# Kernel tuning notes

Measured on AMD Instinct MI355X. Metric: run time of the kernel, lower is better.

## Reference

```python
import jax, jax.numpy as jnp
import numpy as np

B, S, D, H, HD, L, E, K, F = 1, 1024, 1024, 16, 64, 64, 8, 2, 4096
EPS = 1e-6


def rms_norm(x):
    return x / jnp.sqrt(jnp.mean(x * x, axis=-1, keepdims=True) + EPS)


def rope_sincos(seq, dim):
    # standard GPT-NeoX-style rotary tables, shape [seq, dim]
    inv = 1.0 / (10000.0 ** (jnp.arange(0, dim, 2, dtype=jnp.float32) / dim))
    ang = jnp.arange(seq, dtype=jnp.float32)[:, None] * inv[None, :]
    sin = jnp.concatenate([jnp.sin(ang), jnp.sin(ang)], axis=-1)
    cos = jnp.concatenate([jnp.cos(ang), jnp.cos(ang)], axis=-1)
    return sin, cos


def apply_rotary(x, sin, cos):
    d = x.shape[-1] // 2
    rot = jnp.concatenate([-x[..., d:], x[..., :d]], axis=-1)
    return x * cos + rot * sin


def setup_inputs() -> dict:
    key = jax.random.key(0)
    ks = jax.random.split(key, 16)
    sd = 0.02

    def nrm(k, shp):
        return jax.random.normal(k, shp, jnp.float32) * sd

    return dict(
        x=jax.random.normal(ks[0], (B, S, D), jnp.float32),
        noise_u=jax.random.uniform(ks[1], (B, S, E), jnp.float32),
        Wdkv=nrm(ks[2], (H, L, HD)),      # per-head w_dkv  (torch weight [L,HD])
        Wq=nrm(ks[3], (H, HD, HD)),       # per-head wq
        Wuv=nrm(ks[4], (H, L, HD)),       # per-head w_uv
        Wuk=nrm(ks[5], (H, L, HD)),       # per-head w_uk
        Wk_rope=nrm(ks[6], (H, L, HD)),   # per-head w_k_rope
        Wq_rope=nrm(ks[7], (H, HD, L)),   # per-head w_q_rope weight
        bq_rope=jnp.zeros((H, HD), jnp.float32),  # w_q_rope bias (Linear default bias=True)
        Wo_head=nrm(ks[8], (H, HD, HD)),  # per-head w_o (no bias)
        Wr=nrm(ks[9], (E, D)),            # router weight
        Wn=nrm(ks[10], (E, D)),           # noise weight
        r_bias=jnp.zeros((E,), jnp.float32),
        W1=nrm(ks[11], (E, D, F)),        # expert fc1 (transposed torch layout)
        b1=jnp.zeros((E, F), jnp.float32),
        W2=nrm(ks[12], (E, F, D)),        # expert fc2
        b2=jnp.zeros((E, D), jnp.float32),
    )


def reference(x, noise_u, Wdkv, Wq, Wuv, Wuk, Wk_rope, Wq_rope, bq_rope,
              Wo_head, Wr, Wn, r_bias, W1, b1, W2, b2):
    # ---- multi-head latent attention (vectorized over heads) ----
    y = rms_norm(x)
    xs = y.reshape(B, S, H, HD).transpose(0, 2, 1, 3)  # [B,H,S,HD]
    sin_k, cos_k = rope_sincos(S, L)
    sin_q, cos_q = rope_sincos(S, HD)

    k = apply_rotary(jnp.einsum('bhsd,hld->bhsl', xs, Wk_rope), sin_k, cos_k)  # [B,H,S,L]
    ckv = jnp.einsum('bhsd,hld->bhsl', xs, Wdkv)                               # [B,H,S,L]
    q = jnp.einsum('bhsl,hdl->bhsd', ckv, Wq_rope) + bq_rope[None, :, None, :]
    q = apply_rotary(q, sin_q, cos_q)                                          # [B,H,S,HD]

    absorbed = jnp.einsum('hqe,hle->hql', Wq, Wuk)                             # [H,HD,L]
    s1 = jnp.einsum('bhsd,hdl,bhtl->bhst', xs, absorbed, ckv)
    s2 = jnp.einsum('bhsd,bhtd->bhst', q, k)
    scores = (s1 + s2) / jnp.sqrt(jnp.float32(2 * HD))
    mask = jnp.tril(jnp.ones((S, S), dtype=bool))  # past_length = 0
    scores = jnp.where(mask, scores, -jnp.inf)
    attn = jax.nn.softmax(scores, axis=-1)

    v = jnp.einsum('bhsl,hld->bhsd', ckv, Wuv)
    o = jnp.einsum('bhst,bhtd->bhsd', attn, v)
    o = jnp.einsum('bhsd,hed->bhse', o, Wo_head)  # per-head w_o (no bias)
    attn_out = o.transpose(0, 2, 1, 3).reshape(B, S, D)
    x = x + attn_out

    # ---- noisy top-k MoE ----
    y2 = rms_norm(x)
    logits = jnp.einsum('bsd,ed->bse', y2, Wr)
    noisy = jnp.einsum('bsd,ed->bse', y2, Wn)
    nl = noise_u * jax.nn.softplus(noisy) + logits + r_bias
    topv, topi = jax.lax.top_k(nl, K)
    gates = jax.nn.softmax(topv, axis=-1)  # softmax over -inf-scattered logits == softmax over top-k
    probs = jnp.sum(gates[..., None] * jax.nn.one_hot(topi, E, dtype=x.dtype), axis=-2)  # [B,S,E]

    h = jax.nn.gelu(jnp.einsum('bsd,edf->ebsf', y2, W1) + b1[:, None, None, :], approximate=False)
    eo = jnp.einsum('ebsf,efd->ebsd', h, W2) + b2[:, None, None, :]
    moe_out = jnp.einsum('bse,ebsd->bsd', probs, eo)
    return x + moe_out
```

## Files before the change

kernel.cpp:

```cpp
#include <hip/hip_runtime.h>
#include <math.h>

#define S_ 1024
#define D_ 1024
#define H_ 16
#define F_ 4096

typedef short s16x8 __attribute__((ext_vector_type(8)));
typedef float fx4 __attribute__((ext_vector_type(4)));

__device__ __forceinline__ float bf2f(unsigned int u){
  union { float f; unsigned int u; } v; v.u = u<<16; return v.f;
}
__device__ __forceinline__ unsigned short f2bf(float f){
  union { float f; unsigned int u; } v; v.f = f;
  unsigned int r = v.u + 0x7fffu + ((v.u>>16)&1u);
  return (unsigned short)(r>>16);
}
__device__ __forceinline__ unsigned int pk2(float a, float b){
  return (unsigned int)f2bf(a) | ((unsigned int)f2bf(b)<<16);
}
__device__ __forceinline__ void gld16(const void* g, void* l){
  typedef const unsigned int __attribute__((address_space(1)))* gp_t;
  typedef unsigned int __attribute__((address_space(3)))* lp_t;
  __builtin_amdgcn_global_load_lds((gp_t)g, (lp_t)l, 16, 0, 0);
}

__global__ __launch_bounds__(256) void k_rmsnorm(const float* __restrict__ x, unsigned short* __restrict__ y){
  int row = blockIdx.x, t = threadIdx.x;
  const float4 v = ((const float4*)(x + (size_t)row*D_))[t];
  float ss = v.x*v.x + v.y*v.y + v.z*v.z + v.w*v.w;
  #pragma unroll
  for(int o=1;o<64;o<<=1) ss += __shfl_xor(ss, o);
  __shared__ float red[4];
  if((t&63)==0) red[t>>6]=ss;
  __syncthreads();
  float sc = rsqrtf((red[0]+red[1]+red[2]+red[3])*(1.0f/D_) + 1e-6f);
  ushort4 o4;
  o4.x=f2bf(v.x*sc); o4.y=f2bf(v.y*sc); o4.z=f2bf(v.z*sc); o4.w=f2bf(v.w*sc);
  ((ushort4*)(y + (size_t)row*D_))[t]=o4;
}

__global__ __launch_bounds__(256) void k_prep(const float* __restrict__ Wq,
    const float* __restrict__ Wuk, const float* __restrict__ Wuv,
    float* __restrict__ abs_t, float* __restrict__ wuvt){
  int h = blockIdx.x, tid = threadIdx.x;
  __shared__ float wq[4096], wuk[4096];
  for(int i=tid;i<4096;i+=256){ wq[i]=Wq[h*4096+i]; wuk[i]=Wuk[h*4096+i]; }
  __syncthreads();
  for(int i=tid;i<4096;i+=256){
    float a=0.f;
    #pragma unroll 8
    for(int e=0;e<64;e++) a += wq[(i&63)*64+e]*wuk[(i>>6)*64+e];
    abs_t[h*4096+i]=a;
    wuvt[h*4096+i]=Wuv[h*4096 + (i&63)*64 + (i>>6)];
  }
}

__device__ __forceinline__ void stage_B64(const float* __restrict__ W, unsigned short* Bs, int tid){
  int n = tid>>2, kq = tid&3;
  const float* s = W + n*64 + kq*16;
  float4 f0=*(const float4*)(s), f1=*(const float4*)(s+4), f2=*(const float4*)(s+8), f3=*(const float4*)(s+12);
  ushort4 u0,u1,u2,u3;
  u0.x=f2bf(f0.x);u0.y=f2bf(f0.y);u0.z=f2bf(f0.z);u0.w=f2bf(f0.w);
  u1.x=f2bf(f1.x);u1.y=f2bf(f1.y);u1.z=f2bf(f1.z);u1.w=f2bf(f1.w);
  u2.x=f2bf(f2.x);u2.y=f2bf(f2.y);u2.z=f2bf(f2.z);u2.w=f2bf(f2.w);
  u3.x=f2bf(f3.x);u3.y=f2bf(f3.y);u3.z=f2bf(f3.z);u3.w=f2bf(f3.w);
  int sl0=((kq*2)^(n&7))*8, sl1=((kq*2+1)^(n&7))*8;
  *(ushort4*)&Bs[n*64+sl0]=u0;   *(ushort4*)&Bs[n*64+sl0+4]=u1;
  *(ushort4*)&Bs[n*64+sl1]=u2;   *(ushort4*)&Bs[n*64+sl1+4]=u3;
}
__device__ __forceinline__ void gemm64(const unsigned short* Asrc, const unsigned short* Bs,
    int wv, int l16, int l4, fx4 acc[4]){
  int srow = wv*16 + l16;
  #pragma unroll
  for(int kb=0;kb<2;kb++){
    s16x8 af = *(const s16x8*)&Asrc[srow*64 + (((kb*4+l4)^(srow&7))*8)];
    #pragma unroll
    for(int nf=0;nf<4;nf++){
      int n = nf*16+l16;
      s16x8 bf = *(const s16x8*)&Bs[n*64 + (((kb*4+l4)^(n&7))*8)];
      acc[nf] = __builtin_amdgcn_mfma_f32_16x16x32_bf16(af, bf, acc[nf], 0,0,0);
    }
  }
}

__global__ __launch_bounds__(256) void k_proj_m(const unsigned short* __restrict__ y,
    const float* __restrict__ abs_t, const float* __restrict__ wuvt,
    const float* __restrict__ Wdkv, const float* __restrict__ Wk_rope,
    const float* __restrict__ Wq_rope, const float* __restrict__ bq_rope,
    unsigned short* __restrict__ kk, unsigned short* __restrict__ qq,
    unsigned short* __restrict__ vv){
  __shared__ unsigned short ysd[4096];
  __shared__ unsigned short ckvs[4096];
  __shared__ unsigned short Bs[4096];
  __shared__ unsigned short tmp[64*72];
  const float LNC = 0.28782313662425575f;
  const float ASC = 0.08838834764831845f;
  int s0 = blockIdx.x*64, h = blockIdx.y, tid = threadIdx.x;
  int wv = tid>>6, lane = tid&63, l16 = lane&15, l4 = lane>>4;
  fx4 acc[4];

  {
    int rg = lane>>3, sg = (lane&7)^(rg&7);
    #pragma unroll
    for(int c2=0;c2<2;c2++){
      int c = wv*2+c2;
      gld16(y + (size_t)(s0+c*8+rg)*D_ + h*64 + sg*8, &ysd[c*512]);
    }
  }
  stage_B64(Wdkv + h*4096, Bs, tid);
  __syncthreads();

  #pragma unroll
  for(int nf=0;nf<4;nf++){acc[nf][0]=0.f;acc[nf][1]=0.f;acc[nf][2]=0.f;acc[nf][3]=0.f;}
  gemm64(ysd, Bs, wv, l16, l4, acc);
  #pragma unroll
  for(int nf=0;nf<4;nf++){
    int col = nf*16+l16;
    #pragma unroll
    for(int r=0;r<4;r++){
      int srow = wv*16+4*l4+r;
      ckvs[srow*64 + (((col>>3)^(srow&7))*8) + (col&7)] = f2bf(acc[nf][r]);
    }
  }
  __syncthreads();
  {
    int row=tid>>2, sl=(tid&3)*2;
    uint4 a=*(const uint4*)&ckvs[row*64+sl*8];
    uint4 b=*(const uint4*)&ckvs[row*64+sl*8+8];
    unsigned short* kr = kk + ((size_t)(h*S_)+s0+row)*128;
    *(uint4*)&kr[(sl^(row&7))*8]=a;
    *(uint4*)&kr[((sl+1)^(row&7))*8]=b;
  }
  stage_B64(Wk_rope + h*4096, Bs, tid);
  __syncthreads();

  #pragma unroll
  for(int nf=0;nf<4;nf++){acc[nf][0]=0.f;acc[nf][1]=0.f;acc[nf][2]=0.f;acc[nf][3]=0.f;}
  gemm64(ysd, Bs, wv, l16, l4, acc);
  #pragma unroll
  for(int nf=0;nf<2;nf++){
    int llo = nf*16+l16;
    float inv = __expf(-(float)llo * LNC);
    #pragma unroll
    for(int r=0;r<4;r++){
      int srow = wv*16+4*l4+r;
      float sn,cs; __sincosf((float)(s0+srow)*inv,&sn,&cs);
      float alo=acc[nf][r], ahi=acc[nf+2][r];
      tmp[srow*72 + llo]      = f2bf(alo*cs - ahi*sn);
      tmp[srow*72 + llo + 32] = f2bf(ahi*cs + alo*sn);
    }
  }
  __syncthreads();
  { int row=tid>>2, c=(tid&3)*16;
    uint4 a=*(const uint4*)&tmp[row*72+c]; uint4 b=*(const uint4*)&tmp[row*72+c+8];
    unsigned short* kr = kk + ((size_t)(h*S_)+s0+row)*128 + 64;
    *(uint4*)&kr[c]=a; *(uint4*)&kr[c+8]=b; }
  stage_B64(Wq_rope + h*4096, Bs, tid);
  __syncthreads();

  #pragma unroll
  for(int nf=0;nf<4;nf++){acc[nf][0]=0.f;acc[nf][1]=0.f;acc[nf][2]=0.f;acc[nf][3]=0.f;}
  gemm64(ckvs, Bs, wv, l16, l4, acc);
  #pragma unroll
  for(int nf=0;nf<4;nf++){
    float bq = bq_rope[h*64 + nf*16+l16];
    #pragma unroll
    for(int r=0;r<4;r++) acc[nf][r]+=bq;
  }
  #pragma unroll
  for(int nf=0;nf<2;nf++){
    int dlo = nf*16+l16;
    float inv = __expf(-(float)dlo * LNC);
    #pragma unroll
    for(int r=0;r<4;r++){
      int srow = wv*16+4*l4+r;
      float sn,cs; __sincosf((float)(s0+srow)*inv,&sn,&cs);
      float alo=acc[nf][r]*ASC, ahi=acc[nf+2][r]*ASC;
      tmp[srow*72 + dlo]      = f2bf(alo*cs - ahi*sn);
      tmp[srow*72 + dlo + 32] = f2bf(ahi*cs + alo*sn);
    }
  }
  __syncthreads();
  { int row=tid>>2, c=(tid&3)*16;
    uint4 a=*(const uint4*)&tmp[row*72+c]; uint4 b=*(const uint4*)&tmp[row*72+c+8];
    unsigned short* qr = qq + ((size_t)(h*S_)+s0+row)*128 + 64;
    *(uint4*)&qr[c]=a; *(uint4*)&qr[c+8]=b; }
  stage_B64(abs_t + h*4096, Bs, tid);
  __syncthreads();

  #pragma unroll
  for(int nf=0;nf<4;nf++){acc[nf][0]=0.f;acc[nf][1]=0.f;acc[nf][2]=0.f;acc[nf][3]=0.f;}
  gemm64(ysd, Bs, wv, l16, l4, acc);
  #pragma unroll
  for(int nf=0;nf<4;nf++)
    #pragma unroll
    for(int r=0;r<4;r++)
      tmp[(wv*16+4*l4+r)*72 + nf*16+l16] = f2bf(acc[nf][r]*ASC);
  __syncthreads();
  { int row=tid>>2, c=(tid&3)*16;
    uint4 a=*(const uint4*)&tmp[row*72+c]; uint4 b=*(const uint4*)&tmp[row*72+c+8];
    unsigned short* qr = qq + ((size_t)(h*S_)+s0+row)*128;
    *(uint4*)&qr[c]=a; *(uint4*)&qr[c+8]=b; }
  stage_B64(wuvt + h*4096, Bs, tid);
  __syncthreads();

  #pragma unroll
  for(int nf=0;nf<4;nf++){acc[nf][0]=0.f;acc[nf][1]=0.f;acc[nf][2]=0.f;acc[nf][3]=0.f;}
  gemm64(ckvs, Bs, wv, l16, l4, acc);
  #pragma unroll
  for(int nf=0;nf<4;nf++)
    #pragma unroll
    for(int r=0;r<4;r++)
      tmp[(wv*16+4*l4+r)*72 + nf*16+l16] = f2bf(acc[nf][r]);
  __syncthreads();
  { int row=tid>>2, c=(tid&3)*16;
    uint4 a=*(const uint4*)&tmp[row*72+c]; uint4 b=*(const uint4*)&tmp[row*72+c+8];
    unsigned short* vr = vv + ((size_t)(h*S_)+s0+row)*64;
    *(uint4*)&vr[c]=a; *(uint4*)&vr[c+8]=b; }
}

__global__ __launch_bounds__(256) void k_attn2(const unsigned short* __restrict__ qq,
    const unsigned short* __restrict__ kk, const unsigned short* __restrict__ vv,
    const float* __restrict__ Wo, const float* __restrict__ x, float* __restrict__ x1){
  __shared__ unsigned short Ks[64*128];
  __shared__ unsigned short Vt[64*72];
  __shared__ unsigned short Pl[4][16*72];
  int h = blockIdx.y, q0 = blockIdx.x*64, tid = threadIdx.x;
  int wave = tid>>6, lane = tid&63;
  int l16 = lane&15, l4 = lane>>4;
  int qglob = q0 + wave*16 + l16;

  s16x8 qf[4];
  {
    const unsigned short* qp = qq + ((size_t)(h*S_)+qglob)*128 + l4*8;
    #pragma unroll
    for(int kb=0;kb<4;kb++) qf[kb] = *(const s16x8*)(qp + kb*32);
  }
  fx4 ot[4];
  #pragma unroll
  for(int t=0;t<4;t++){ ot[t][0]=0.f; ot[t][1]=0.f; ot[t][2]=0.f; ot[t][3]=0.f; }
  float mrun=-1e30f, lrun=0.f;
  int nkt = blockIdx.x + 1;

  for(int kt=0;kt<nkt;kt++){
    int kt0 = kt*64;
    __syncthreads();
    #pragma unroll
    for(int it=0;it<4;it++){
      int idx = tid + it*256;
      int row = idx>>4, c = idx&15;
      uint4 u = *(const uint4*)(kk + ((size_t)(h*S_)+kt0+row)*128 + c*8);
      *(uint4*)&Ks[row*128 + ((c^(row&7))<<3)] = u;
    }
    #pragma unroll
    for(int it=0;it<2;it++){
      int idx = tid + it*256;
      int k = idx>>3, d0 = (idx&7)*8;
      uint4 u = *(const uint4*)(vv + ((size_t)(h*S_)+kt0+k)*64 + d0);
      unsigned short t8[8];
      *(uint4*)t8 = u;
      #pragma unroll
      for(int j=0;j<8;j++) Vt[(d0+j)*72 + k] = t8[j];
    }
    __syncthreads();

    fx4 sa[4];
    #pragma unroll
    for(int i=0;i<4;i++){ sa[i][0]=0.f; sa[i][1]=0.f; sa[i][2]=0.f; sa[i][3]=0.f; }
    #pragma unroll
    for(int kb=0;kb<4;kb++){
      #pragma unroll
      for(int i=0;i<4;i++){
        int row = 16*i + l16;
        s16x8 ak = *(const s16x8*)&Ks[row*128 + (((l4+4*kb)^(row&7))<<3)];
        sa[i] = __builtin_amdgcn_mfma_f32_16x16x32_bf16(ak, qf[kb], sa[i], 0,0,0);
      }
    }
    float pv[16]; float mloc=-1e30f;
    #pragma unroll
    for(int i=0;i<4;i++)
      #pragma unroll
      for(int r=0;r<4;r++){
        int kg = kt0 + 16*i + 4*l4 + r;
        float s = (kg<=qglob)? sa[i][r] : -1e30f;
        pv[i*4+r]=s; mloc=fmaxf(mloc,s);
      }
    mloc = fmaxf(mloc, __shfl_xor(mloc,16));
    mloc = fmaxf(mloc, __shfl_xor(mloc,32));
    float mnew = fmaxf(mrun,mloc);
    float alpha = __expf(mrun-mnew);
    float psum=0.f;
    #pragma unroll
    for(int z=0;z<16;z++){ pv[z]=__expf(pv[z]-mnew); psum+=pv[z]; }
    psum += __shfl_xor(psum,16); psum += __shfl_xor(psum,32);
    lrun = lrun*alpha + psum; mrun = mnew;
    #pragma unroll
    for(int t=0;t<4;t++){ ot[t][0]*=alpha; ot[t][1]*=alpha; ot[t][2]*=alpha; ot[t][3]*=alpha; }
    {
      unsigned short* pw = &Pl[wave][l16*72 + 4*l4];
      #pragma unroll
      for(int i=0;i<4;i++){
        *(unsigned int*)&pw[16*i]   = pk2(pv[i*4+0],pv[i*4+1]);
        *(unsigned int*)&pw[16*i+2] = pk2(pv[i*4+2],pv[i*4+3]);
      }
    }
    #pragma unroll
    for(int kb=0;kb<2;kb++){
      s16x8 pf = *(const s16x8*)&Pl[wave][l16*72 + kb*32 + l4*8];
      #pragma unroll
      for(int t=0;t<4;t++){
        s16x8 av = *(const s16x8*)&Vt[(16*t+l16)*72 + kb*32 + l4*8];
        ot[t] = __builtin_amdgcn_mfma_f32_16x16x32_bf16(av, pf, ot[t], 0,0,0);
      }
    }
  }

  float invl = 1.f/lrun;
  {
    unsigned short* pw = &Pl[wave][l16*72 + 4*l4];
    #pragma unroll
    for(int t=0;t<4;t++){
      *(unsigned int*)&pw[16*t]   = pk2(ot[t][0]*invl, ot[t][1]*invl);
      *(unsigned int*)&pw[16*t+2] = pk2(ot[t][2]*invl, ot[t][3]*invl);
    }
  }
  __syncthreads();
  #pragma unroll
  for(int it=0;it<4;it++){
    int idx = tid + it*256;
    int ee = idx>>4, dd = (idx&15)*4;
    float4 wv = *(const float4*)(Wo + h*4096 + ee*64 + dd);
    ushort4 w4; w4.x=f2bf(wv.x); w4.y=f2bf(wv.y); w4.z=f2bf(wv.z); w4.w=f2bf(wv.w);
    *(ushort4*)&Vt[ee*72 + dd] = w4;
  }
  __syncthreads();
  fx4 outT[4];
  #pragma unroll
  for(int t=0;t<4;t++){ outT[t][0]=0.f; outT[t][1]=0.f; outT[t][2]=0.f; outT[t][3]=0.f; }
  #pragma unroll
  for(int kb=0;kb<2;kb++){
    s16x8 of = *(const s16x8*)&Pl[wave][l16*72 + kb*32 + l4*8];
    #pragma unroll
    for(int t=0;t<4;t++){
      s16x8 aw = *(const s16x8*)&Vt[(16*t+l16)*72 + kb*32 + l4*8];
      outT[t] = __builtin_amdgcn_mfma_f32_16x16x32_bf16(aw, of, outT[t], 0,0,0);
    }
  }
  #pragma unroll
  for(int t=0;t<4;t++){
    size_t base = (size_t)qglob*D_ + h*64 + 16*t + 4*l4;
    float4 xv = *(const float4*)(x + base);
    float4 r;
    r.x = xv.x + outT[t][0]; r.y = xv.y + outT[t][1];
    r.z = xv.z + outT[t][2]; r.w = xv.w + outT[t][3];
    *(float4*)(x1+base) = r;
  }
}

__global__ __launch_bounds__(64) void k_gate(const float* __restrict__ x1, const float* __restrict__ Wr,
    const float* __restrict__ Wn, const float* __restrict__ r_bias, const float* __restrict__ noise_u,
    float* __restrict__ gates, int* __restrict__ topi){
  int s = blockIdx.x, lane = threadIdx.x;
  const float* xr = x1 + (size_t)s*D_ + lane*16;
  float yv[16]; float ss=0.f;
  #pragma unroll
  for(int i=0;i<16;i+=4){
    float4 a = *(const float4*)(xr+i);
    yv[i]=a.x; yv[i+1]=a.y; yv[i+2]=a.z; yv[i+3]=a.w;
    ss += a.x*a.x+a.y*a.y+a.z*a.z+a.w*a.w;
  }
  #pragma unroll
  for(int o=1;o<64;o<<=1) ss += __shfl_xor(ss,o);
  float sc = rsqrtf(ss*(1.0f/D_) + 1e-6f);
  #pragma unroll
  for(int i=0;i<16;i++) yv[i]*=sc;
  float lg[8], nz[8];
  #pragma unroll
  for(int e=0;e<8;e++){
    const float* wr = Wr + e*D_ + lane*16;
    const float* wn = Wn + e*D_ + lane*16;
    float a=0.f,b=0.f;
    #pragma unroll
    for(int i=0;i<16;i+=4){
      float4 w1 = *(const float4*)(wr+i); float4 w2 = *(const float4*)(wn+i);
      a += yv[i]*w1.x + yv[i+1]*w1.y + yv[i+2]*w1.z + yv[i+3]*w1.w;
      b += yv[i]*w2.x + yv[i+1]*w2.y + yv[i+2]*w2.z + yv[i+3]*w2.w;
    }
    lg[e]=a; nz[e]=b;
  }
  #pragma unroll
  for(int o=1;o<64;o<<=1){
    #pragma unroll
    for(int e=0;e<8;e++){ lg[e]+=__shfl_xor(lg[e],o); nz[e]+=__shfl_xor(nz[e],o); }
  }
  if(lane==0){
    float nl[8];
    for(int e=0;e<8;e++){
      float z = nz[e];
      float sp = (z>20.f)? z : log1pf(expf(z));
      nl[e] = noise_u[s*8+e]*sp + lg[e] + r_bias[e];
    }
    int i0=0; float v0=nl[0];
    for(int e=1;e<8;e++) if(nl[e]>v0){v0=nl[e];i0=e;}
    float v1=-1e30f; int i1=0;
    for(int e=0;e<8;e++) if(e!=i0 && nl[e]>v1){v1=nl[e];i1=e;}
    float ex = expf(v1-v0);
    gates[s*2]   = 1.f/(1.f+ex);
    gates[s*2+1] = ex/(1.f+ex);
    topi[s*2]=i0; topi[s*2+1]=i1;
  }
}

__global__ __launch_bounds__(256) void k_lists(const int* __restrict__ topi,
    int* __restrict__ offs, int* __restrict__ pair_tok, int* __restrict__ slot_of){
  __shared__ int tp[2048];
  __shared__ int cnt[8];
  __shared__ int off_s[9];
  int t = threadIdx.x;
  int wave = t>>6, lane = t&63;
  unsigned long long below = (lane==63)? 0xFFFFFFFFFFFFFFFFull>>1
                                       : ((1ull<<lane)-1ull);
  for(int i=t;i<2048;i+=256) tp[i]=topi[i];
  __syncthreads();
  #pragma unroll
  for(int sub=0;sub<2;sub++){
    int e = wave*2+sub;
    int c=0;
    for(int ch=0;ch<32;ch++) c += (tp[ch*64+lane]==e);
    #pragma unroll
    for(int o=1;o<64;o<<=1) c += __shfl_xor(c,o);
    if(lane==0) cnt[e]=c;
  }
  __syncthreads();
  if(t==0){
    int a=0;
    for(int e=0;e<8;e++){ off_s[e]=a; a += (cnt[e]+127)&~127; }
    off_s[8]=a;
    for(int e=0;e<9;e++) offs[e]=off_s[e];
  }
  __syncthreads();
  #pragma unroll
  for(int sub=0;sub<2;sub++){
    int e = wave*2+sub;
    int base = off_s[e];
    for(int ch=0;ch<32;ch++){
      int idx = ch*64+lane;
      bool pred = (tp[idx]==e);
      unsigned long long mask = __ballot(pred);
      if(pred){
        int slot = base + __popcll(mask & below);
        pair_tok[slot] = idx>>1;
        slot_of[idx] = slot;
      }
      base += __popcll(mask);
    }
    for(int slot=base+lane; slot<off_s[e+1]; slot+=64) pair_tok[slot]=0;
  }
}

__global__ __launch_bounds__(256) void k_cvt_t(const float* __restrict__ src,
    unsigned short* __restrict__ dst, int R, int C){
  __shared__ float ts[64][65];
  int e = blockIdx.z;
  int r0 = blockIdx.x*64, c0 = blockIdx.y*64;
  const float* s = src + (size_t)e*R*C;
  unsigned short* d = dst + (size_t)e*R*C;
  int t = threadIdx.x;
  #pragma unroll
  for(int it=0; it<4; it++){
    int flat = it*256+t;
    int r = flat>>4, cq = (flat&15)*4;
    float4 v = *(const float4*)(s + (size_t)(r0+r)*C + c0+cq);
    ts[r][cq]=v.x; ts[r][cq+1]=v.y; ts[r][cq+2]=v.z; ts[r][cq+3]=v.w;
  }
  __syncthreads();
  #pragma unroll
  for(int it=0; it<4; it++){
    int flat = it*256+t;
    int c = flat>>4, kq = (flat&15)*4;
    ushort4 o;
    o.x=f2bf(ts[kq][c]); o.y=f2bf(ts[kq+1][c]); o.z=f2bf(ts[kq+2][c]); o.w=f2bf(ts[kq+3][c]);
    *(ushort4*)(d + (size_t)(c0+c)*R + r0+kq) = o;
  }
}

__global__ __launch_bounds__(256) void k_fc1t(const unsigned short* __restrict__ y2,
    const int* __restrict__ pair_tok, const int* __restrict__ offs,
    const unsigned short* __restrict__ Bt, const float* __restrict__ bias1,
    unsigned short* __restrict__ hbuf){
  __shared__ unsigned short As[128*64];
  __shared__ unsigned short Bs[128*64];
  __shared__ int sh_e;
  int tid=threadIdx.x, lane=tid&63, wv=tid>>6;
  int r0=blockIdx.x*128, n0=blockIdx.y*128;
  if(tid==0){ int e=-1; if(r0<offs[8]){e=0; while(offs[e+1]<=r0) e++;} sh_e=e; }
  __syncthreads();
  int e=sh_e; if(e<0) return;
  int rg = lane>>3;
  int sg = (lane&7)^(rg&7);
  const unsigned short* aptr[4];
  const unsigned short* bptr[4];
  #pragma unroll
  for(int c=0;c<4;c++){
    int ch = wv*4+c;
    int tok = pair_tok[r0 + ch*8 + rg];
    aptr[c] = y2 + (size_t)tok*D_ + sg*8;
    bptr[c] = Bt + (size_t)e*D_*F_ + (size_t)(n0 + ch*8 + rg)*D_ + sg*8;
  }
  int l16=lane&15, l4=lane>>4;
  int wm=wv>>1, wn=wv&1;
  fx4 acc[4][4];
  #pragma unroll
  for(int a0=0;a0<4;a0++)
    #pragma unroll
    for(int b0=0;b0<4;b0++){ acc[a0][b0][0]=0.f; acc[a0][b0][1]=0.f; acc[a0][b0][2]=0.f; acc[a0][b0][3]=0.f; }

  for(int kt=0;kt<D_;kt+=64){
    __syncthreads();
    #pragma unroll
    for(int c=0;c<4;c++){
      gld16(aptr[c]+kt, &As[(wv*4+c)*512]);
      gld16(bptr[c]+kt, &Bs[(wv*4+c)*512]);
    }
    __syncthreads();
    #pragma unroll
    for(int kb=0;kb<2;kb++){
      s16x8 af[4], bf8[4];
      #pragma unroll
      for(int mf=0;mf<4;mf++){
        int row = wm*64+mf*16+l16;
        af[mf] = *(const s16x8*)&As[row*64 + (((kb*4+l4)^(row&7))*8)];
      }
      #pragma unroll
      for(int nf=0;nf<4;nf++){
        int col = wn*64+nf*16+l16;
        bf8[nf] = *(const s16x8*)&Bs[col*64 + (((kb*4+l4)^(col&7))*8)];
      }
      #pragma unroll
      for(int mf=0;mf<4;mf++)
        #pragma unroll
        for(int nf=0;nf<4;nf++)
          acc[mf][nf]=__builtin_amdgcn_mfma_f32_16x16x32_bf16(af[mf],bf8[nf],acc[mf][nf],0,0,0);
    }
  }
  #pragma unroll
  for(int mf=0;mf<4;mf++)
    #pragma unroll
    for(int nf=0;nf<4;nf++){
      int gcol=n0+wn*64+nf*16+l16;
      float bias=bias1[e*F_+gcol];
      #pragma unroll
      for(int rgi=0;rgi<4;rgi++){
        int grow=r0+wm*64+mf*16+l4*4+rgi;
        float vv=acc[mf][nf][rgi]+bias;
        float g=0.5f*vv*(1.f+erff(vv*0.70710678118654752f));
        hbuf[(size_t)grow*F_+gcol]=f2bf(g);
      }
    }
}

__global__ __launch_bounds__(256) void k_fc2t(const unsigned short* __restrict__ hbuf,
    const int* __restrict__ offs, const unsigned short* __restrict__ Bt,
    const float* __restrict__ bias2, float* __restrict__ eo, int klen){
  __shared__ unsigned short As[128*64];
  __shared__ unsigned short Bs[64*64];
  __shared__ int sh_e;
  int tid=threadIdx.x, lane=tid&63, wv=tid>>6;
  int r0=blockIdx.x*128, n0=blockIdx.y*64;
  int k0=blockIdx.z*klen;
  if(tid==0){ int e=-1; if(r0<offs[8]){e=0; while(offs[e+1]<=r0) e++;} sh_e=e; }
  __syncthreads();
  int e=sh_e; if(e<0) return;
  int rg = lane>>3;
  int sg = (lane&7)^(rg&7);
  const unsigned short* aptr[4];
  const unsigned short* bptr[2];
  #pragma unroll
  for(int c=0;c<4;c++){
    int ch = wv*4+c;
    aptr[c] = hbuf + (size_t)(r0 + ch*8 + rg)*F_ + k0 + sg*8;
  }
  #pragma unroll
  for(int c=0;c<2;c++){
    int ch = wv*2+c;
    bptr[c] = Bt + (size_t)e*F_*D_ + (size_t)(n0 + ch*8 + rg)*F_ + k0 + sg*8;
  }
  int l16=lane&15, l4=lane>>4;
  fx4 acc[2][4];
  #pragma unroll
  for(int a0=0;a0<2;a0++)
    #pragma unroll
    for(int b0=0;b0<4;b0++){ acc[a0][b0][0]=0.f; acc[a0][b0][1]=0.f; acc[a0][b0][2]=0.f; acc[a0][b0][3]=0.f; }

  for(int kt=0;kt<klen;kt+=64){
    __syncthreads();
    #pragma unroll
    for(int c=0;c<4;c++) gld16(aptr[c]+kt, &As[(wv*4+c)*512]);
    #pragma unroll
    for(int c=0;c<2;c++) gld16(bptr[c]+kt, &Bs[(wv*2+c)*512]);
    __syncthreads();
    #pragma unroll
    for(int kb=0;kb<2;kb++){
      s16x8 af[2], bf8[4];
      #pragma unroll
      for(int mf=0;mf<2;mf++){
        int row = wv*32+mf*16+l16;
        af[mf] = *(const s16x8*)&As[row*64 + (((kb*4+l4)^(row&7))*8)];
      }
      #pragma unroll
      for(int nf=0;nf<4;nf++){
        int col = nf*16+l16;
        bf8[nf] = *(const s16x8*)&Bs[col*64 + (((kb*4+l4)^(col&7))*8)];
      }
      #pragma unroll
      for(int mf=0;mf<2;mf++)
        #pragma unroll
        for(int nf=0;nf<4;nf++)
          acc[mf][nf]=__builtin_amdgcn_mfma_f32_16x16x32_bf16(af[mf],bf8[nf],acc[mf][nf],0,0,0);
    }
  }
  float* eop = eo + (size_t)blockIdx.z*3072*D_;
  #pragma unroll
  for(int mf=0;mf<2;mf++)
    #pragma unroll
    for(int nf=0;nf<4;nf++){
      int gcol=n0+nf*16+l16;
      float bias=(blockIdx.z==0)? bias2[e*D_+gcol] : 0.f;
      #pragma unroll
      for(int rgi=0;rgi<4;rgi++){
        int grow=r0+wv*32+mf*16+l4*4+rgi;
        eop[(size_t)grow*D_+gcol]=acc[mf][nf][rgi]+bias;
      }
    }
}

__global__ __launch_bounds__(256) void k_fc1_fb(const unsigned short* __restrict__ y2,
    const int* __restrict__ pair_tok, const int* __restrict__ offs,
    const float* __restrict__ W1, const float* __restrict__ bias1,
    unsigned short* __restrict__ hbuf){
  __shared__ unsigned short As[4096];
  __shared__ unsigned short Bs[4096];
  __shared__ int sh_e;
  int tid=threadIdx.x;
  int r0=blockIdx.x*128, n0=blockIdx.y*128;
  if(tid==0){ int e=-1; if(r0<offs[8]){ e=0; while(offs[e+1]<=r0) e++; } sh_e=e; }
  __syncthreads();
  int e=sh_e; if(e<0) return;
  const float* Bsrc = W1 + (size_t)e*D_*F_;
  int r=tid&127, hf=tid>>7;
  int tok=pair_tok[r0+r];
  const unsigned short* Asrc = y2 + (size_t)tok*D_ + hf*16;
  int pk=tid>>5, pn=tid&31;
  int lane=tid&63, wvid=tid>>6;
  int wm=wvid>>1, wn=wvid&1;
  int l16=lane&15, l4=lane>>4;
  fx4 acc[4][4];
  #pragma unroll
  for(int a0=0;a0<4;a0++)
    #pragma unroll
    for(int b0=0;b0<4;b0++){ acc[a0][b0][0]=0.f; acc[a0][b0][1]=0.f; acc[a0][b0][2]=0.f; acc[a0][b0][3]=0.f; }
  for(int kt=0;kt<D_;kt+=32){
    uint4 av0=*(const uint4*)(Asrc+kt);
    uint4 av1=*(const uint4*)(Asrc+kt+8);
    const float* bp=Bsrc+(size_t)(kt+pk*4)*F_+n0+pn*4;
    float4 bv0=*(const float4*)(bp);
    float4 bv1=*(const float4*)(bp+F_);
    float4 bv2=*(const float4*)(bp+2*F_);
    float4 bv3=*(const float4*)(bp+3*F_);
    *(uint4*)&As[(hf*2)*1024 + r*8]=av0;
    *(uint4*)&As[(hf*2+1)*1024 + r*8]=av1;
    unsigned short c0[4]={f2bf(bv0.x),f2bf(bv0.y),f2bf(bv0.z),f2bf(bv0.w)};
    unsigned short c1[4]={f2bf(bv1.x),f2bf(bv1.y),f2bf(bv1.z),f2bf(bv1.w)};
    unsigned short c2[4]={f2bf(bv2.x),f2bf(bv2.y),f2bf(bv2.z),f2bf(bv2.w)};
    unsigned short c3[4]={f2bf(bv3.x),f2bf(bv3.y),f2bf(bv3.z),f2bf(bv3.w)};
    #pragma unroll
    for(int j2=0;j2<4;j2++){
      int col=pn*4+j2;
      int kb=(pk*4)^(((col>>2)&3)<<3);
      ushort4 wr;
      wr.x=c0[j2]; wr.y=c1[j2]; wr.z=c2[j2]; wr.w=c3[j2];
      *(ushort4*)&Bs[col*32+kb]=wr;
    }
    __syncthreads();
    s16x8 af[4],bf8[4];
    #pragma unroll
    for(int mf=0;mf<4;mf++){
      int rowl=wm*64+mf*16+l16;
      af[mf]=*(const s16x8*)&As[l4*1024+rowl*8];
    }
    #pragma unroll
    for(int nf=0;nf<4;nf++){
      int col=wn*64+nf*16+l16;
      int kb=(l4*8)^(((col>>2)&3)<<3);
      bf8[nf]=*(const s16x8*)&Bs[col*32+kb];
    }
    #pragma unroll
    for(int mf=0;mf<4;mf++)
      #pragma unroll
      for(int nf=0;nf<4;nf++)
        acc[mf][nf]=__builtin_amdgcn_mfma_f32_16x16x32_bf16(af[mf],bf8[nf],acc[mf][nf],0,0,0);
    __syncthreads();
  }
  #pragma unroll
  for(int mf=0;mf<4;mf++)
    #pragma unroll
    for(int nf=0;nf<4;nf++){
      int gcol=n0+wn*64+nf*16+l16;
      float bias=bias1[e*F_+gcol];
      #pragma unroll
      for(int rg=0;rg<4;rg++){
        int grow=r0+wm*64+mf*16+l4*4+rg;
        float vv=acc[mf][nf][rg]+bias;
        float g=0.5f*vv*(1.f+erff(vv*0.70710678118654752f));
        hbuf[(size_t)grow*F_+gcol]=f2bf(g);
      }
    }
}

__global__ __launch_bounds__(256) void k_fc2_fb(const unsigned short* __restrict__ hbuf,
    const int* __restrict__ offs, const float* __restrict__ W2,
    const float* __restrict__ bias2, float* __restrict__ eo){
  __shared__ unsigned short As[4096];
  __shared__ unsigned short Bs[2048];
  __shared__ int sh_e;
  int tid=threadIdx.x;
  int r0=blockIdx.x*128, n0=blockIdx.y*64;
  if(tid==0){ int e=-1; if(r0<offs[8]){ e=0; while(offs[e+1]<=r0) e++; } sh_e=e; }
  __syncthreads();
  int e=sh_e; if(e<0) return;
  const float* Bsrc=W2+(size_t)e*F_*D_;
  int r=tid&127, hf=tid>>7;
  const unsigned short* Asrc=hbuf+(size_t)(r0+r)*F_+hf*16;
  int pk=tid>>4, pn=tid&15;
  int lane=tid&63, wvid=tid>>6;
  int l16=lane&15, l4=lane>>4;
  fx4 acc[2][4];
  #pragma unroll
  for(int a0=0;a0<2;a0++)
    #pragma unroll
    for(int b0=0;b0<4;b0++){ acc[a0][b0][0]=0.f; acc[a0][b0][1]=0.f; acc[a0][b0][2]=0.f; acc[a0][b0][3]=0.f; }
  for(int kt=0;kt<F_;kt+=32){
    uint4 av0=*(const uint4*)(Asrc+kt);
    uint4 av1=*(const uint4*)(Asrc+kt+8);
    const float* bp=Bsrc+(size_t)(kt+pk*2)*D_+n0+pn*4;
    float4 bv0=*(const float4*)bp;
    float4 bv1=*(const float4*)(bp+D_);
    *(uint4*)&As[(hf*2)*1024+r*8]=av0;
    *(uint4*)&As[(hf*2+1)*1024+r*8]=av1;
    unsigned short c0[4]={f2bf(bv0.x),f2bf(bv0.y),f2bf(bv0.z),f2bf(bv0.w)};
    unsigned short c1[4]={f2bf(bv1.x),f2bf(bv1.y),f2bf(bv1.z),f2bf(bv1.w)};
    #pragma unroll
    for(int j2=0;j2<4;j2++){
      int col=pn*4+j2;
      int kb=(pk*2)^(((col>>2)&3)<<3);
      unsigned int pack=(unsigned int)c0[j2] | ((unsigned int)c1[j2]<<16);
      *(unsigned int*)&Bs[col*32+kb]=pack;
    }
    __syncthreads();
    s16x8 af[2],bf8[4];
    #pragma unroll
    for(int mf=0;mf<2;mf++){
      int rowl=wvid*32+mf*16+l16;
      af[mf]=*(const s16x8*)&As[l4*1024+rowl*8];
    }
    #pragma unroll
    for(int nf=0;nf<4;nf++){
      int col=nf*16+l16;
      int kb=(l4*8)^(((col>>2)&3)<<3);
      bf8[nf]=*(const s16x8*)&Bs[col*32+kb];
    }
    #pragma unroll
    for(int mf=0;mf<2;mf++)
      #pragma unroll
      for(int nf=0;nf<4;nf++)
        acc[mf][nf]=__builtin_amdgcn_mfma_f32_16x16x32_bf16(af[mf],bf8[nf],acc[mf][nf],0,0,0);
    __syncthreads();
  }
  #pragma unroll
  for(int mf=0;mf<2;mf++)
    #pragma unroll
    for(int nf=0;nf<4;nf++){
      int gcol=n0+nf*16+l16;
      float bias=bias2[e*D_+gcol];
      #pragma unroll
      for(int rg=0;rg<4;rg++){
        int grow=r0+wvid*32+mf*16+l4*4+rg;
        eo[(size_t)grow*D_+gcol]=acc[mf][nf][rg]+bias;
      }
    }
}

__global__ __launch_bounds__(256) void k_combine(const float* __restrict__ x1, const float* __restrict__ eo,
    int parts, const float* __restrict__ gates, const int* __restrict__ slot_of, float* __restrict__ out){
  int s=blockIdx.x, t=threadIdx.x;
  float g0=gates[s*2], g1=gates[s*2+1];
  int a0=slot_of[s*2], a1=slot_of[s*2+1];
  float4 o=((const float4*)(x1+(size_t)s*D_))[t];
  for(int p=0;p<parts;p++){
    const float* ep = eo + (size_t)p*3072*D_;
    float4 e0=((const float4*)(ep+(size_t)a0*D_))[t];
    float4 e1=((const float4*)(ep+(size_t)a1*D_))[t];
    o.x+=g0*e0.x+g1*e1.x;
    o.y+=g0*e0.y+g1*e1.y;
    o.z+=g0*e0.z+g1*e1.z;
    o.w+=g0*e0.w+g1*e1.w;
  }
  ((float4*)(out+(size_t)s*D_))[t]=o;
}

extern "C" void kernel_launch(void* const* d_in, const int* in_sizes, int n_in,
                              void* d_out, int out_size, void* d_ws, size_t ws_size,
                              hipStream_t stream){
  (void)in_sizes; (void)n_in; (void)out_size;
  const float* x       = (const float*)d_in[0];
  const float* noise_u = (const float*)d_in[1];
  const float* Wdkv    = (const float*)d_in[2];
  const float* Wq      = (const float*)d_in[3];
  const float* Wuv     = (const float*)d_in[4];
  const float* Wuk     = (const float*)d_in[5];
  const float* Wk_rope = (const float*)d_in[6];
  const float* Wq_rope = (const float*)d_in[7];
  const float* bq_rope = (const float*)d_in[8];
  const float* Wo_head = (const float*)d_in[9];
  const float* Wr      = (const float*)d_in[10];
  const float* Wn      = (const float*)d_in[11];
  const float* r_bias  = (const float*)d_in[12];
  const float* W1      = (const float*)d_in[13];
  const float* b1      = (const float*)d_in[14];
  const float* W2      = (const float*)d_in[15];
  const float* b2      = (const float*)d_in[16];
  float* out           = (float*)d_out;

  char* w = (char*)d_ws;
  unsigned short* y    = (unsigned short*)(w);
  unsigned short* kk   = (unsigned short*)(w + 2097152);
  unsigned short* qq   = (unsigned short*)(w + 6291456);
  unsigned short* vv   = (unsigned short*)(w + 10485760);
  float* abs_t         = (float*)(w + 12582912);
  float* wuvt          = (float*)(w + 12845056);
  float* x1            = (float*)(w + 13107200);
  unsigned short* y2   = (unsigned short*)(w + 17301504);
  float* gates         = (float*)(w + 19398656);
  int* topi            = (int*)(w + 19406848);
  int* slot_of         = (int*)(w + 19415040);
  int* offs            = (int*)(w + 19423232);
  int* pair_tok        = (int*)(w + 19427328);
  unsigned short* hbuf = (unsigned short*)(w + 19443712);
  float* eo            = (float*)(w + 44609536);

  const size_t NEED4 = 162050048ull;
  const size_t NEED2 = 136884224ull;
  int parts; unsigned short* Wt;
  if(ws_size >= NEED4){ parts = 4; Wt = (unsigned short*)(w + 94941184); }
  else if(ws_size >= NEED2){ parts = 2; Wt = (unsigned short*)(w + 69775360); }
  else { parts = 0; Wt = 0; }

  if(parts){
    k_cvt_t<<<dim3(16,64,8),256,0,stream>>>(W1, Wt, D_, F_);
  }
  k_rmsnorm<<<S_,256,0,stream>>>(x, y);
  k_prep<<<H_,256,0,stream>>>(Wq, Wuk, Wuv, abs_t, wuvt);
  k_proj_m<<<dim3(16,H_),256,0,stream>>>(y, abs_t, wuvt, Wdkv, Wk_rope, Wq_rope, bq_rope, kk, qq, vv);
  k_attn2<<<dim3(16,H_),256,0,stream>>>(qq, kk, vv, Wo_head, x, x1);
  k_rmsnorm<<<S_,256,0,stream>>>(x1, y2);
  k_gate<<<S_,64,0,stream>>>(x1, Wr, Wn, r_bias, noise_u, gates, topi);
  k_lists<<<1,256,0,stream>>>(topi, offs, pair_tok, slot_of);
  if(parts){
    k_fc1t<<<dim3(24,32),256,0,stream>>>(y2, pair_tok, offs, Wt, b1, hbuf);
    k_cvt_t<<<dim3(64,16,8),256,0,stream>>>(W2, Wt, F_, D_);
    k_fc2t<<<dim3(24,16,parts),256,0,stream>>>(hbuf, offs, Wt, b2, eo, F_/parts);
    k_combine<<<S_,256,0,stream>>>(x1, eo, parts, gates, slot_of, out);
  } else {
    k_fc1_fb<<<dim3(24,32),256,0,stream>>>(y2, pair_tok, offs, W1, b1, hbuf);
    k_fc2_fb<<<dim3(24,16),256,0,stream>>>(hbuf, offs, W2, b2, eo);
    k_combine<<<S_,256,0,stream>>>(x1, eo, 1, gates, slot_of, out);
  }
}
```

Baseline: 309.8 us.

## Double-buffer LDS tiles in MoE FC1/FC2 GEMMs to overlap loads with MFMA

Each expert GEMM kernel now keeps two LDS buffers for its A and B tiles and issues the direct-to-LDS loads for the next K step before computing the current one. Explicit vmcnt waits and raw s_barrier replace the paired __syncthreads, so global-load latency can be hidden behind the MFMA work. LDS use per block doubles, which may lower occupancy. Correctness depends on the hand-written wait counts matching the number of outstanding loads, and on the asm barriers ordering LDS reads with later writes.

```diff
diff --git a/kernel.cpp b/kernel.cpp
--- a/kernel.cpp
+++ b/kernel.cpp
@@ -125,8 +125,7 @@
     }
   }
   __syncthreads();
-  {
-    int row=tid>>2, sl=(tid&3)*2;
+  { int row=tid>>2, sl=(tid&3)*2;
     uint4 a=*(const uint4*)&ckvs[row*64+sl*8];
     uint4 b=*(const uint4*)&ckvs[row*64+sl*8+8];
     unsigned short* kr = kk + ((size_t)(h*S_)+s0+row)*128;
@@ -490,8 +489,8 @@
     const int* __restrict__ pair_tok, const int* __restrict__ offs,
     const unsigned short* __restrict__ Bt, const float* __restrict__ bias1,
     unsigned short* __restrict__ hbuf){
-  __shared__ unsigned short As[128*64];
-  __shared__ unsigned short Bs[128*64];
+  __shared__ unsigned short As[2][8192];
+  __shared__ unsigned short Bs[2][8192];
   __shared__ int sh_e;
   int tid=threadIdx.x, lane=tid&63, wv=tid>>6;
   int r0=blockIdx.x*128, n0=blockIdx.y*128;
@@ -517,26 +516,33 @@
     #pragma unroll
     for(int b0=0;b0<4;b0++){ acc[a0][b0][0]=0.f; acc[a0][b0][1]=0.f; acc[a0][b0][2]=0.f; acc[a0][b0][3]=0.f; }
 
-  for(int kt=0;kt<D_;kt+=64){
-    __syncthreads();
+  #pragma unroll
+  for(int c=0;c<4;c++){
+    gld16(aptr[c], &As[0][(wv*4+c)*512]);
+    gld16(bptr[c], &Bs[0][(wv*4+c)*512]);
+  }
+
+  int buf=0;
+  for(int kt=0;kt<D_-64;kt+=64){
     #pragma unroll
     for(int c=0;c<4;c++){
-      gld16(aptr[c]+kt, &As[(wv*4+c)*512]);
-      gld16(bptr[c]+kt, &Bs[(wv*4+c)*512]);
-    }
-    __syncthreads();
+      gld16(aptr[c]+kt+64, &As[buf^1][(wv*4+c)*512]);
+      gld16(bptr[c]+kt+64, &Bs[buf^1][(wv*4+c)*512]);
+    }
+    asm volatile("s_waitcnt vmcnt(8)" ::: "memory");
+    asm volatile("s_barrier" ::: "memory");
     #pragma unroll
     for(int kb=0;kb<2;kb++){
       s16x8 af[4], bf8[4];
       #pragma unroll
       for(int mf=0;mf<4;mf++){
         int row = wm*64+mf*16+l16;
-        af[mf] = *(const s16x8*)&As[row*64 + (((kb*4+l4)^(row&7))*8)];
+        af[mf] = *(const s16x8*)&As[buf][row*64 + (((kb*4+l4)^(row&7))*8)];
       }
       #pragma unroll
       for(int nf=0;nf<4;nf++){
         int col = wn*64+nf*16+l16;
-        bf8[nf] = *(const s16x8*)&Bs[col*64 + (((kb*4+l4)^(col&7))*8)];
+        bf8[nf] = *(const s16x8*)&Bs[buf][col*64 + (((kb*4+l4)^(col&7))*8)];
       }
       #pragma unroll
       for(int mf=0;mf<4;mf++)
@@ -544,6 +550,29 @@
         for(int nf=0;nf<4;nf++)
           acc[mf][nf]=__builtin_amdgcn_mfma_f32_16x16x32_bf16(af[mf],bf8[nf],acc[mf][nf],0,0,0);
     }
+    asm volatile("s_barrier" ::: "memory");
+    buf ^= 1;
+  }
+  asm volatile("s_waitcnt vmcnt(0)" ::: "memory");
+  asm volatile("s_barrier" ::: "memory");
+  #pragma unroll
+  for(int kb=0;kb<2;kb++){
+    s16x8 af[4], bf8[4];
+    #pragma unroll
+    for(int mf=0;mf<4;mf++){
+      int row = wm*64+mf*16+l16;
+      af[mf] = *(const s16x8*)&As[buf][row*64 + (((kb*4+l4)^(row&7))*8)];
+    }
+    #pragma unroll
+    for(int nf=0;nf<4;nf++){
+      int col = wn*64+nf*16+l16;
+      bf8[nf] = *(const s16x8*)&Bs[buf][col*64 + (((kb*4+l4)^(col&7))*8)];
+    }
+    #pragma unroll
+    for(int mf=0;mf<4;mf++)
+      #pragma unroll
+      for(int nf=0;nf<4;nf++)
+        acc[mf][nf]=__builtin_amdgcn_mfma_f32_16x16x32_bf16(af[mf],bf8[nf],acc[mf][nf],0,0,0);
   }
   #pragma unroll
   for(int mf=0;mf<4;mf++)
@@ -564,8 +593,8 @@
 __global__ __launch_bounds__(256) void k_fc2t(const unsigned short* __restrict__ hbuf,
     const int* __restrict__ offs, const unsigned short* __restrict__ Bt,
     const float* __restrict__ bias2, float* __restrict__ eo, int klen){
-  __shared__ unsigned short As[128*64];
-  __shared__ unsigned short Bs[64*64];
+  __shared__ unsigned short As[2][8192];
+  __shared__ unsigned short Bs[2][4096];
   __shared__ int sh_e;
   int tid=threadIdx.x, lane=tid&63, wv=tid>>6;
   int r0=blockIdx.x*128, n0=blockIdx.y*64;
@@ -594,25 +623,31 @@
     #pragma unroll
     for(int b0=0;b0<4;b0++){ acc[a0][b0][0]=0.f; acc[a0][b0][1]=0.f; acc[a0][b0][2]=0.f; acc[a0][b0][3]=0.f; }
 
-  for(int kt=0;kt<klen;kt+=64){
-    __syncthreads();
-    #pragma unroll
-    for(int c=0;c<4;c++) gld16(aptr[c]+kt, &As[(wv*4+c)*512]);
-    #pragma unroll
-    for(int c=0;c<2;c++) gld16(bptr[c]+kt, &Bs[(wv*2+c)*512]);
-    __syncthreads();
+  #pragma unroll
+  for(int c=0;c<4;c++) gld16(aptr[c], &As[0][(wv*4+c)*512]);
+  #pragma unroll
+  for(int c=0;c<2;c++) gld16(bptr[c], &Bs[0][(wv*2+c)*512]);
+
+  int buf=0;
+  for(int kt=0;kt<klen-64;kt+=64){
+    #pragma unroll
+    for(int c=0;c<4;c++) gld16(aptr[c]+kt+64, &As[buf^1][(wv*4+c)*512]);
+    #pragma unroll
+    for(int c=0;c<2;c++) gld16(bptr[c]+kt+64, &Bs[buf^1][(wv*2+c)*512]);
+    asm volatile("s_waitcnt vmcnt(6)" ::: "memory");
+    asm volatile("s_barrier" ::: "memory");
     #pragma unroll
     for(int kb=0;kb<2;kb++){
       s16x8 af[2], bf8[4];
       #pragma unroll
       for(int mf=0;mf<2;mf++){
         int row = wv*32+mf*16+l16;
-        af[mf] = *(const s16x8*)&As[row*64 + (((kb*4+l4)^(row&7))*8)];
+        af[mf] = *(const s16x8*)&As[buf][row*64 + (((kb*4+l4)^(row&7))*8)];
       }
       #pragma unroll
       for(int nf=0;nf<4;nf++){
         int col = nf*16+l16;
-        bf8[nf] = *(const s16x8*)&Bs[col*64 + (((kb*4+l4)^(col&7))*8)];
+        bf8[nf] = *(const s16x8*)&Bs[buf][col*64 + (((kb*4+l4)^(col&7))*8)];
       }
       #pragma unroll
       for(int mf=0;mf<2;mf++)
@@ -620,6 +655,29 @@
         for(int nf=0;nf<4;nf++)
           acc[mf][nf]=__builtin_amdgcn_mfma_f32_16x16x32_bf16(af[mf],bf8[nf],acc[mf][nf],0,0,0);
     }
+    asm volatile("s_barrier" ::: "memory");
+    buf ^= 1;
+  }
+  asm volatile("s_waitcnt vmcnt(0)" ::: "memory");
+  asm volatile("s_barrier" ::: "memory");
+  #pragma unroll
+  for(int kb=0;kb<2;kb++){
+    s16x8 af[2], bf8[4];
+    #pragma unroll
+    for(int mf=0;mf<2;mf++){
+      int row = wv*32+mf*16+l16;
+      af[mf] = *(const s16x8*)&As[buf][row*64 + (((kb*4+l4)^(row&7))*8)];
+    }
+    #pragma unroll
+    for(int nf=0;nf<4;nf++){
+      int col = nf*16+l16;
+      bf8[nf] = *(const s16x8*)&Bs[buf][col*64 + (((kb*4+l4)^(col&7))*8)];
+    }
+    #pragma unroll
+    for(int mf=0;mf<2;mf++)
+      #pragma unroll
+      for(int nf=0;nf<4;nf++)
+        acc[mf][nf]=__builtin_amdgcn_mfma_f32_16x16x32_bf16(af[mf],bf8[nf],acc[mf][nf],0,0,0);
   }
   float* eop = eo + (size_t)blockIdx.z*3072*D_;
   #pragma unroll
```

Result: slower. 318.7 us (+2.8%).
